# Performance work log

Hardware: AMD Instinct MI355X
Metric: run time of the kernel (lower is better)

The kernel has to match this reference:

```python
import jax, jax.numpy as jnp
import numpy as np

T, S, N, E, H, FF = 1024, 2048, 4, 1024, 16, 4096
HD = E // H
EPS = 1e-5


def layer_norm(x, g, b):
    mu = jnp.mean(x, axis=-1, keepdims=True)
    var = jnp.mean(jnp.square(x - mu), axis=-1, keepdims=True)
    return (x - mu) / jnp.sqrt(var + EPS) * g + b


def mha(q_in, k_in, v_in, w_in, b_in, w_out, b_out):
    # q_in: (T,N,E), k_in/v_in: (S,N,E); matches torch F.linear with (3E,E) weight
    t, n, e = q_in.shape
    s = k_in.shape[0]
    wq, wk, wv = jnp.split(w_in, 3, axis=0)
    bq, bk, bv = jnp.split(b_in, 3)
    q = (q_in @ wq.T + bq) * (HD ** -0.5)
    k = k_in @ wk.T + bk
    v = v_in @ wv.T + bv
    # (L,N,E) -> (N*H, L, HD)
    q = q.reshape(t, n * H, HD).transpose(1, 0, 2)
    k = k.reshape(s, n * H, HD).transpose(1, 0, 2)
    v = v.reshape(s, n * H, HD).transpose(1, 0, 2)
    attn = jax.nn.softmax(jnp.einsum('bth,bsh->bts', q, k), axis=-1)
    out = jnp.einsum('bts,bsh->bth', attn, v)  # (N*H, T, HD)
    out = out.transpose(1, 0, 2).reshape(t, n, e)
    return out @ w_out.T + b_out


def setup_inputs() -> dict:
    key = jax.random.key(0)
    ks = jax.random.split(key, 16)
    p = lambda k, shape: jax.random.normal(k, shape, dtype=jnp.float32) * 0.02
    return {
        'tgt': jax.random.normal(ks[0], (T, N, E), dtype=jnp.float32),
        'memory': jax.random.normal(ks[1], (S, N, E), dtype=jnp.float32),
        'sa_w_in': p(ks[2], (3 * E, E)), 'sa_b_in': jnp.zeros((3 * E,), jnp.float32),
        'sa_w_out': p(ks[3], (E, E)), 'sa_b_out': jnp.zeros((E,), jnp.float32),
        'ca_w_in': p(ks[4], (3 * E, E)), 'ca_b_in': jnp.zeros((3 * E,), jnp.float32),
        'ca_w_out': p(ks[5], (E, E)), 'ca_b_out': jnp.zeros((E,), jnp.float32),
        'w1': p(ks[6], (FF, E)), 'b1': jnp.zeros((FF,), jnp.float32),
        'w2': p(ks[7], (E, FF)), 'b2': jnp.zeros((E,), jnp.float32),
        'ln1_g': jnp.ones((E,), jnp.float32), 'ln1_b': jnp.zeros((E,), jnp.float32),
        'ln2_g': jnp.ones((E,), jnp.float32), 'ln2_b': jnp.zeros((E,), jnp.float32),
        'ln3_g': jnp.ones((E,), jnp.float32), 'ln3_b': jnp.zeros((E,), jnp.float32),
    }


def reference(tgt, memory, sa_w_in, sa_b_in, sa_w_out, sa_b_out,
              ca_w_in, ca_b_in, ca_w_out, ca_b_out,
              w1, b1, w2, b2, ln1_g, ln1_b, ln2_g, ln2_b, ln3_g, ln3_b):
    # self-attention block (post-LN residual); dropout = identity (eval mode)
    tgt2 = mha(tgt, tgt, tgt, sa_w_in, sa_b_in, sa_w_out, sa_b_out)
    x = layer_norm(tgt + tgt2, ln1_g, ln1_b)
    # cross-attention block
    tgt2 = mha(x, memory, memory, ca_w_in, ca_b_in, ca_w_out, ca_b_out)
    x = layer_norm(x + tgt2, ln2_g, ln2_b)
    # FFN with relu
    tgt2 = jax.nn.relu(x @ w1.T + b1) @ w2.T + b2
    return layer_norm(x + tgt2, ln3_g, ln3_b)
```

## Files before the change

kernel.cpp:

```cpp
#include <hip/hip_runtime.h>


typedef __bf16 bf16x8 __attribute__((ext_vector_type(8)));
typedef float  f32x4  __attribute__((ext_vector_type(4)));
typedef float  f32x16 __attribute__((ext_vector_type(16)));

#define T_  1024
#define S_  2048
#define NB_ 4
#define E_  1024
#define H_  16
#define HD_ 64
#define FF_ 4096
#define M1_ (T_*NB_)
#define M2_ (S_*NB_)
#define LOG2E 1.44269504088896f

__device__ __forceinline__ unsigned short f2bf(float f){
  unsigned int u = __builtin_bit_cast(unsigned int, f);
  u += 0x7fffu + ((u>>16)&1u);
  return (unsigned short)(u>>16);
}
__device__ __forceinline__ float bf2f(unsigned short h){
  unsigned int u = ((unsigned int)h)<<16;
  return __builtin_bit_cast(float, u);
}

__device__ __forceinline__ void gload16(unsigned short* l, const unsigned short* g){
  __builtin_amdgcn_global_load_lds(
      (const __attribute__((address_space(1))) unsigned int*)g,
      (__attribute__((address_space(3))) unsigned int*)l, 16, 0, 0);
}

__device__ __forceinline__ void perm32swap(unsigned &a, unsigned &b){
  asm("v_permlane32_swap_b32 %0, %1" : "+v"(a), "+v"(b));
}

struct CvtSeg { const float* s; unsigned short* d; int n4; };
struct CvtArgs { CvtSeg seg[8]; int blk_end[8]; };
__global__ __launch_bounds__(256) void f2b_multi_k(CvtArgs a){
  const int b = blockIdx.x;
  int si = 0;
  #pragma unroll
  for (int i=0;i<8;i++) if (b >= a.blk_end[i]) si = i+1;
  const int base = si ? a.blk_end[si-1] : 0;
  const int i4 = (b - base)*256 + threadIdx.x;
  if (i4 >= a.seg[si].n4) return;
  float4 f = ((const float4*)a.seg[si].s)[i4];
  union { unsigned short u[4]; uint2 v; } t;
  t.u[0]=f2bf(f.x); t.u[1]=f2bf(f.y); t.u[2]=f2bf(f.z); t.u[3]=f2bf(f.w);
  ((uint2*)a.seg[si].d)[i4] = t.v;
}

template<int FLAGS, int BN>
__global__ __launch_bounds__(256) void gemm_k(
    const unsigned short* __restrict__ A, int lda,
    const unsigned short* __restrict__ B, int ldb,
    const float* __restrict__ bias,
    const float* __restrict__ res,
    unsigned short* __restrict__ Cb, float* __restrict__ Cf,
    int M, int N, int K)
{
  constexpr int NW = BN/32;
  __shared__ unsigned short a_sh[128*64];
  __shared__ unsigned short b_sh[BN*64];
  const int tid  = threadIdx.x;
  const int wave = tid>>6;
  const int lane = tid&63;
  const int l15 = lane&15, l4 = lane>>4;
  const int row0 = blockIdx.x*128, col0 = blockIdx.y*BN;
  const int wm = (wave>>1)*64, wn = (wave&1)*(BN/2);

  const int lrow = tid>>3;
  const int scol = ((tid&7) ^ (lrow&7)) << 3;
  const int dst8 = (tid&7) << 3;

  f32x4 acc[4][NW] = {};

  for (int k0=0; k0<K; k0+=64){
    const unsigned short* ga = A + (size_t)(row0+lrow)*lda + k0 + scol;
    const unsigned short* gb = B + (size_t)(col0+lrow)*ldb + k0 + scol;
    #pragma unroll
    for (int i=0;i<4;i++)
      gload16(&a_sh[(lrow + i*32)*64 + dst8], ga + (size_t)(i*32)*lda);
    #pragma unroll
    for (int i=0;i<BN/32;i++)
      gload16(&b_sh[(lrow + i*32)*64 + dst8], gb + (size_t)(i*32)*ldb);
    __syncthreads();
    #pragma unroll
    for (int kk=0;kk<2;kk++){
      const int sw = (((kk<<2)|l4) ^ (l15&7)) << 3;
      bf16x8 af[4], bfr[NW];
      #pragma unroll
      for (int m=0;m<4;m++)  af[m]  = *(const bf16x8*)&a_sh[(wm + m*16 + l15)*64 + sw];
      #pragma unroll
      for (int n=0;n<NW;n++) bfr[n] = *(const bf16x8*)&b_sh[(wn + n*16 + l15)*64 + sw];
      #pragma unroll
      for (int m=0;m<4;m++)
        #pragma unroll
        for (int n=0;n<NW;n++)
          acc[m][n] = __builtin_amdgcn_mfma_f32_16x16x32_bf16(af[m], bfr[n], acc[m][n], 0,0,0);
    }
    __syncthreads();
  }

  #pragma unroll
  for (int m=0;m<4;m++){
    #pragma unroll
    for (int r=0;r<4;r++){
      const int rr = row0 + wm + m*16 + l4*4 + r;
      #pragma unroll
      for (int n=0;n<NW;n++){
        const int cc = col0 + wn + n*16 + l15;
        float v = acc[m][n][r] + bias[cc];
        if (FLAGS & 1) v = fmaxf(v, 0.f);
        if (FLAGS & 2) v += res[(size_t)rr*N + cc];
        if (FLAGS & 4) Cb[(size_t)rr*N + cc] = f2bf(v);
        if (FLAGS & 8) Cf[(size_t)rr*N + cc] = v;
      }
    }
  }
}

template<int BN>
__global__ __launch_bounds__(256) void gemm_splitk_k(
    const unsigned short* __restrict__ A, int lda,
    const unsigned short* __restrict__ B, int ldb,
    const float* __restrict__ bias,
    const float* __restrict__ res,
    float* __restrict__ P0, float* __restrict__ P1,
    int M, int N, int K)
{
  constexpr int NW = BN/32;
  __shared__ unsigned short a_sh[128*64];
  __shared__ unsigned short b_sh[BN*64];
  const int tid  = threadIdx.x;
  const int wave = tid>>6;
  const int lane = tid&63;
  const int l15 = lane&15, l4 = lane>>4;
  const int row0 = blockIdx.x*128, col0 = blockIdx.y*BN;
  const int wm = (wave>>1)*64, wn = (wave&1)*(BN/2);
  const int z = blockIdx.z;
  const int kh = K>>1;
  const int kbeg = z*kh;

  const int lrow = tid>>3;
  const int scol = ((tid&7) ^ (lrow&7)) << 3;
  const int dst8 = (tid&7) << 3;

  f32x4 acc[4][NW] = {};

  for (int k0=kbeg; k0<kbeg+kh; k0+=64){
    const unsigned short* ga = A + (size_t)(row0+lrow)*lda + k0 + scol;
    const unsigned short* gb = B + (size_t)(col0+lrow)*ldb + k0 + scol;
    #pragma unroll
    for (int i=0;i<4;i++)
      gload16(&a_sh[(lrow + i*32)*64 + dst8], ga + (size_t)(i*32)*lda);
    #pragma unroll
    for (int i=0;i<BN/32;i++)
      gload16(&b_sh[(lrow + i*32)*64 + dst8], gb + (size_t)(i*32)*ldb);
    __syncthreads();
    #pragma unroll
    for (int kk=0;kk<2;kk++){
      const int sw = (((kk<<2)|l4) ^ (l15&7)) << 3;
      bf16x8 af[4], bfr[NW];
      #pragma unroll
      for (int m=0;m<4;m++)  af[m]  = *(const bf16x8*)&a_sh[(wm + m*16 + l15)*64 + sw];
      #pragma unroll
      for (int n=0;n<NW;n++) bfr[n] = *(const bf16x8*)&b_sh[(wn + n*16 + l15)*64 + sw];
      #pragma unroll
      for (int m=0;m<4;m++)
        #pragma unroll
        for (int n=0;n<NW;n++)
          acc[m][n] = __builtin_amdgcn_mfma_f32_16x16x32_bf16(af[m], bfr[n], acc[m][n], 0,0,0);
    }
    __syncthreads();
  }

  float* out = z ? P1 : P0;
  #pragma unroll
  for (int m=0;m<4;m++){
    #pragma unroll
    for (int r=0;r<4;r++){
      const int rr = row0 + wm + m*16 + l4*4 + r;
      #pragma unroll
      for (int n=0;n<NW;n++){
        const int cc = col0 + wn + n*16 + l15;
        float v = acc[m][n][r];
        if (!z) v += bias[cc] + res[(size_t)rr*N + cc];
        out[(size_t)rr*N + cc] = v;
      }
    }
  }
}

template<int BN>
__global__ __launch_bounds__(256) void gemm_scat_k(
    const unsigned short* __restrict__ A, int lda,
    const unsigned short* __restrict__ B, int ldb,
    const float* __restrict__ bias,
    unsigned short* __restrict__ qb, unsigned short* __restrict__ kb,
    unsigned short* __restrict__ vtb,
    int M, int N, int K, int nq, int nk, int Lq, int Lkv, float qscale)
{
  constexpr int NW = BN/32;
  constexpr int SMEM_ELEMS = (BN==128) ? (128*132) : (128*64 + BN*64);
  __shared__ unsigned short smem[SMEM_ELEMS];
  unsigned short* a_sh = smem;
  unsigned short* b_sh = smem + 128*64;
  const int tid  = threadIdx.x;
  const int wave = tid>>6, lane = tid&63;
  const int l15 = lane&15, l4 = lane>>4;
  const int row0 = blockIdx.x*128, col0 = blockIdx.y*BN;
  const int wm = (wave>>1)*64, wn = (wave&1)*(BN/2);

  const int lrow = tid>>3;
  const int scol = ((tid&7) ^ (lrow&7)) << 3;
  const int dst8 = (tid&7) << 3;

  f32x4 acc[4][NW] = {};

  for (int k0=0; k0<K; k0+=64){
    const unsigned short* ga = A + (size_t)(row0+lrow)*lda + k0 + scol;
    const unsigned short* gb = B + (size_t)(col0+lrow)*ldb + k0 + scol;
    #pragma unroll
    for (int i=0;i<4;i++)
      gload16(&a_sh[(lrow + i*32)*64 + dst8], ga + (size_t)(i*32)*lda);
    #pragma unroll
    for (int i=0;i<BN/32;i++)
      gload16(&b_sh[(lrow + i*32)*64 + dst8], gb + (size_t)(i*32)*ldb);
    __syncthreads();
    #pragma unroll
    for (int kk=0;kk<2;kk++){
      const int sw = (((kk<<2)|l4) ^ (l15&7)) << 3;
      bf16x8 af[4], bfr[NW];
      #pragma unroll
      for (int m=0;m<4;m++)  af[m]  = *(const bf16x8*)&a_sh[(wm + m*16 + l15)*64 + sw];
      #pragma unroll
      for (int n=0;n<NW;n++) bfr[n] = *(const bf16x8*)&b_sh[(wn + n*16 + l15)*64 + sw];
      #pragma unroll
      for (int m=0;m<4;m++)
        #pragma unroll
        for (int n=0;n<NW;n++)
          acc[m][n] = __builtin_amdgcn_mfma_f32_16x16x32_bf16(af[m], bfr[n], acc[m][n], 0,0,0);
    }
    __syncthreads();
  }

  if (col0 < nq + nk){
    const bool isq = (col0 < nq);
    unsigned short* dst = isq ? qb : kb;
    const int  base  = isq ? 0 : nq;
    const int  L     = isq ? Lq : Lkv;
    const float scale = isq ? qscale : 1.0f;
    #pragma unroll
    for (int m=0;m<4;m++){
      #pragma unroll
      for (int r=0;r<4;r++){
        const int rr = row0 + wm + m*16 + l4*4 + r;
        const int t = rr>>2, nn = rr&3;
        #pragma unroll
        for (int n=0;n<NW;n++){
          const int cc = col0 + wn + n*16 + l15;
          const int e = cc - base, h = e>>6, d = e&63;
          const float v = (acc[m][n][r] + bias[cc]) * scale;
          dst[((size_t)(nn*H_ + h)*L + t)*HD_ + d] = f2bf(v);
        }
      }
    }
  } else if constexpr (BN == 128){
    unsigned short* cT = smem;
    #pragma unroll
    for (int m=0;m<4;m++){
      const int tl = ((wm + m*16)>>2) + l4;
      #pragma unroll
      for (int n=0;n<4;n++){
        const int ccl = wn + n*16 + l15;
        const float bi = bias[col0 + ccl];
        #pragma unroll
        for (int r=0;r<4;r++)
          cT[ccl*132 + r*32 + tl] = f2bf(acc[m][n][r] + bi);
      }
    }
    __syncthreads();
    const int t0 = row0>>2;
    const int tl4 = tid&7, c5 = tid>>3;
    const int voff = nq + nk;
    #pragma unroll
    for (int i=0;i<16;i++){
      const int combo = i*32 + c5;
      const int nn = combo&3, ccl = combo>>2;
      const int e = col0 + ccl - voff, h = e>>6, d = e&63;
      const uint2 val = *(const uint2*)&cT[ccl*132 + nn*32 + tl4*4];
      *(uint2*)(vtb + (size_t)((nn*H_ + h)*HD_ + d)*Lkv + t0 + tl4*4) = val;
    }
  }
}

template<bool PARTIAL, int NT>
__global__ __launch_bounds__(256,3) void attn_k(
    const unsigned short* __restrict__ qb, const unsigned short* __restrict__ kb,
    const unsigned short* __restrict__ vtb,
    unsigned short* __restrict__ o_out, float* __restrict__ l_out,
    int T, int S)
{
  static_assert((NT & 1) == 0 && NT >= 4, "NT even");
  __shared__ unsigned short k_sh[2][64*64];
  __shared__ unsigned short v_sh[2][64*64];
  __shared__ float bc_sh[4][32];
  const int tid  = threadIdx.x;
  const int wave = tid>>6, lane = tid&63;
  const int l31  = lane&31;
  const int hv   = lane>>5;
  const int bh   = blockIdx.x;
  const int z    = blockIdx.z;
  const int s_begin = z * (NT*64);
  const int q0   = blockIdx.y*128 + wave*32;
  const size_t qbase = (size_t)bh*T*HD_;
  const size_t kbase = (size_t)bh*S*HD_;
  const size_t vbase = (size_t)bh*HD_*S;

  const int strow = tid>>3;
  const int stch  = tid&7;
  const int sc_sw = (stch ^ (strow&7)) << 3;
  const int dst8  = stch<<3;
  const unsigned short* gk0 = kb  + kbase + (size_t)s_begin*HD_;
  const unsigned short* gv0 = vtb + vbase + s_begin;

  auto stageK = [&](int t, int slot){
    const unsigned short* g = gk0 + (size_t)(t*64)*HD_;
    gload16(&k_sh[slot][(strow   )*64 + dst8], g + (size_t)(strow   )*HD_ + sc_sw);
    gload16(&k_sh[slot][(strow+32)*64 + dst8], g + (size_t)(strow+32)*HD_ + sc_sw);
  };
  auto stageV = [&](int t, int slot){
    const unsigned short* g = gv0 + t*64;
    gload16(&v_sh[slot][(strow   )*64 + dst8], g + (size_t)(strow   )*S + sc_sw);
    gload16(&v_sh[slot][(strow+32)*64 + dst8], g + (size_t)(strow+32)*S + sc_sw);
  };

  bf16x8 qf[4];
  #pragma unroll
  for (int p=0;p<4;p++)
    qf[p] = *(const bf16x8*)(qb + qbase + (size_t)(q0 + l31)*HD_ + p*16 + hv*8);
  asm volatile("" ::: "memory");

  stageK(0, 0);

  f32x16 o0 = {}, o1 = {};
  float rsa = 0.f, rsb = 0.f;
  bf16x8 paA[4], paB[4];

  auto QK = [&](const unsigned short* ksh, f32x16& s0, f32x16& s1){
    #pragma unroll
    for (int p=0;p<4;p++){
      const int slot = 2*p + hv;
      bf16x8 kf0 = *(const bf16x8*)&ksh[(l31     )*64 + ((slot ^ (l31&7))<<3)];
      bf16x8 kf1 = *(const bf16x8*)&ksh[(l31 + 32)*64 + ((slot ^ (l31&7))<<3)];
      s0 = __builtin_amdgcn_mfma_f32_32x32x16_bf16(kf0, qf[p], s0, 0,0,0);
      s1 = __builtin_amdgcn_mfma_f32_32x32x16_bf16(kf1, qf[p], s1, 0,0,0);
    }
  };
  auto PV = [&](const unsigned short* vsh, const bf16x8* pa){
    #pragma unroll
    for (int ks=0;ks<4;ks++){
      const int slot = 2*ks + hv;
      bf16x8 vf0 = *(const bf16x8*)&vsh[(l31     )*64 + ((slot ^ (l31&7))<<3)];
      bf16x8 vf1 = *(const bf16x8*)&vsh[(l31 + 32)*64 + ((slot ^ (l31&7))<<3)];
      o0 = __builtin_amdgcn_mfma_f32_32x32x16_bf16(pa[ks], vf0, o0, 0,0,0);
      o1 = __builtin_amdgcn_mfma_f32_32x32x16_bf16(pa[ks], vf1, o1, 0,0,0);
    }
  };
  auto SM = [&](f32x16& s0, f32x16& s1, bf16x8* pa){
    #pragma unroll
    for (int r=0;r<16;r++){
      s0[r] = __builtin_amdgcn_exp2f(s0[r]);
      s1[r] = __builtin_amdgcn_exp2f(s1[r]);
    }
    #pragma unroll
    for (int r=0;r<16;r+=2){
      rsa += s0[r]   + s1[r];
      rsb += s0[r+1] + s1[r+1];
    }
    #pragma unroll
    for (int ks=0;ks<4;ks++){
      const int base = 8*(ks&1);
      unsigned pkA0, pkA1, pkB0, pkB1;
      if (ks < 2){
        asm("v_cvt_pk_bf16_f32 %0, %1, %2" : "=v"(pkA0) : "v"(s0[base+0]), "v"(s0[base+1]));
        asm("v_cvt_pk_bf16_f32 %0, %1, %2" : "=v"(pkA1) : "v"(s0[base+2]), "v"(s0[base+3]));
        asm("v_cvt_pk_bf16_f32 %0, %1, %2" : "=v"(pkB0) : "v"(s0[base+4]), "v"(s0[base+5]));
        asm("v_cvt_pk_bf16_f32 %0, %1, %2" : "=v"(pkB1) : "v"(s0[base+6]), "v"(s0[base+7]));
      } else {
        asm("v_cvt_pk_bf16_f32 %0, %1, %2" : "=v"(pkA0) : "v"(s1[base+0]), "v"(s1[base+1]));
        asm("v_cvt_pk_bf16_f32 %0, %1, %2" : "=v"(pkA1) : "v"(s1[base+2]), "v"(s1[base+3]));
        asm("v_cvt_pk_bf16_f32 %0, %1, %2" : "=v"(pkB0) : "v"(s1[base+4]), "v"(s1[base+5]));
        asm("v_cvt_pk_bf16_f32 %0, %1, %2" : "=v"(pkB1) : "v"(s1[base+6]), "v"(s1[base+7]));
      }
      perm32swap(pkA0, pkB0);
      perm32swap(pkA1, pkB1);
      union { unsigned w[4]; bf16x8 v; } u;
      u.w[0] = pkA0; u.w[1] = pkA1; u.w[2] = pkB0; u.w[3] = pkB1;
      pa[ks] = u.v;
    }
  };

  {
    stageK(1, 1);
    stageV(0, 0);
    asm volatile("s_waitcnt vmcnt(4)" ::: "memory");
    __builtin_amdgcn_s_barrier();
    f32x16 s0 = {}, s1 = {};
    __builtin_amdgcn_s_setprio(1);
    QK(k_sh[0], s0, s1);
    __builtin_amdgcn_s_setprio(0);
    SM(s0, s1, paA);
    __builtin_amdgcn_s_barrier();
  }

  auto BODY = [&](int i, const bf16x8* paPrev, bf16x8* paCur){
    const int kt = (i+1 < NT) ? (i+1) : (NT-1);
    stageK(kt, (i+1)&1);
    stageV(i, i&1);
    asm volatile("s_waitcnt vmcnt(4)" ::: "memory");
    __builtin_amdgcn_s_barrier();
    f32x16 s0 = {}, s1 = {};
    __builtin_amdgcn_s_setprio(1);
    QK(k_sh[i&1], s0, s1);
    PV(v_sh[(i+1)&1], paPrev);
    __builtin_amdgcn_s_setprio(0);
    SM(s0, s1, paCur);
    __builtin_amdgcn_s_barrier();
  };

  for (int ii=1; ii+1<NT; ii+=2){
    BODY(ii,   paA, paB);
    BODY(ii+1, paB, paA);
  }
  BODY(NT-1, paA, paB);

  asm volatile("s_waitcnt vmcnt(0)" ::: "memory");
  __builtin_amdgcn_s_barrier();
  __builtin_amdgcn_s_setprio(1);
  PV(v_sh[(NT-1)&1], paB);
  __builtin_amdgcn_s_setprio(0);

  float l_run = rsa + rsb;
  {
    unsigned a_ = __builtin_bit_cast(unsigned, l_run), b_ = a_;
    perm32swap(a_, b_);
    l_run += __builtin_bit_cast(float, hv ? a_ : b_);
  }

  if constexpr (PARTIAL){
    const size_t obase = (size_t)(z*64 + bh)*T;
    #pragma unroll
    for (int r=0;r<16;r++){
      const int qr = (r&3) + 8*(r>>2) + 4*hv;
      unsigned short* op = o_out + (obase + q0 + qr)*HD_;
      op[l31]      = f2bf(o0[r]);
      op[l31 + 32] = f2bf(o1[r]);
    }
    if (hv == 0) l_out[obase + q0 + l31] = l_run;
  } else {
    bc_sh[wave][l31] = 1.f / l_run;
    const int nb = bh>>4, hh = bh&15;
    #pragma unroll
    for (int r=0;r<16;r++){
      const int qr  = (r&3) + 8*(r>>2) + 4*hv;
      const float inv = bc_sh[wave][qr];
      const int t = q0 + qr;
      unsigned short* op = o_out + ((size_t)t*NB_ + nb)*E_ + hh*HD_;
      op[l31]      = f2bf(o0[r]*inv);
      op[l31 + 32] = f2bf(o1[r]*inv);
    }
  }
}

__global__ __launch_bounds__(256) void comb_k(
    const unsigned short* __restrict__ opart, const float* __restrict__ lpart,
    unsigned short* __restrict__ outb, int T)
{
  const int bh = blockIdx.y;
  const int t  = blockIdx.x*4 + (threadIdx.x>>6);
  const int d  = threadIdx.x&63;
  const size_t half = (size_t)64*T;
  const size_t row  = (size_t)bh*T + t;
  const float o = bf2f(opart[row*HD_ + d]) + bf2f(opart[(half + row)*HD_ + d]);
  const float l = lpart[row] + lpart[half + row];
  const int nb = bh>>4, hh = bh&15;
  outb[((size_t)t*NB_ + nb)*E_ + hh*HD_ + d] = f2bf(o / l);
}

__global__ __launch_bounds__(256) void ln_k(
    const float* __restrict__ p0, const float* __restrict__ p1,
    const float* __restrict__ g, const float* __restrict__ bb,
    float* __restrict__ of, unsigned short* __restrict__ ob)
{
  const int row = blockIdx.x, tid = threadIdx.x;
  const size_t base = (size_t)row*E_;
  float v[4];
  #pragma unroll
  for (int i=0;i<4;i++){
    const int col = tid + 256*i;
    v[i] = p0[base + col] + p1[base + col];
  }
  float s  = v[0]+v[1]+v[2]+v[3];
  float s2 = v[0]*v[0]+v[1]*v[1]+v[2]*v[2]+v[3]*v[3];
  #pragma unroll
  for (int off=32; off>0; off>>=1){
    s  += __shfl_down(s, off);
    s2 += __shfl_down(s2, off);
  }
  __shared__ float red[8];
  if ((tid&63)==0){ red[tid>>6] = s; red[4+(tid>>6)] = s2; }
  __syncthreads();
  s  = red[0]+red[1]+red[2]+red[3];
  s2 = red[4]+red[5]+red[6]+red[7];
  const float mu   = s * (1.f/E_);
  const float var  = s2 * (1.f/E_) - mu*mu;
  const float rstd = rsqrtf(var + 1e-5f);
  #pragma unroll
  for (int i=0;i<4;i++){
    const int col = tid + 256*i;
    const float y = (v[i]-mu)*rstd*g[col] + bb[col];
    if (of) of[base + col] = y;
    if (ob) ob[base + col] = f2bf(y);
  }
}

extern "C" void kernel_launch(void* const* d_in, const int* in_sizes, int n_in,
                              void* d_out, int out_size, void* d_ws, size_t ws_size,
                              hipStream_t stream)
{
  const float* tgt      = (const float*)d_in[0];
  const float* mem      = (const float*)d_in[1];
  const float* sa_w_in  = (const float*)d_in[2];
  const float* sa_b_in  = (const float*)d_in[3];
  const float* sa_w_out = (const float*)d_in[4];
  const float* sa_b_out = (const float*)d_in[5];
  const float* ca_w_in  = (const float*)d_in[6];
  const float* ca_b_in  = (const float*)d_in[7];
  const float* ca_w_out = (const float*)d_in[8];
  const float* ca_b_out = (const float*)d_in[9];
  const float* w1 = (const float*)d_in[10];
  const float* b1 = (const float*)d_in[11];
  const float* w2 = (const float*)d_in[12];
  const float* b2 = (const float*)d_in[13];
  const float* ln1_g=(const float*)d_in[14]; const float* ln1_b=(const float*)d_in[15];
  const float* ln2_g=(const float*)d_in[16]; const float* ln2_b=(const float*)d_in[17];
  const float* ln3_g=(const float*)d_in[18]; const float* ln3_b=(const float*)d_in[19];

  char* ws = (char*)d_ws;
  size_t off = 0;
  auto alloc = [&](size_t bytes)->char* {
    char* p = ws + off; off += (bytes + 255) & ~(size_t)255; return p;
  };
  unsigned short* w_sa_in_b  = (unsigned short*)alloc((size_t)3*E_*E_*2);
  unsigned short* w_sa_out_b = (unsigned short*)alloc((size_t)E_*E_*2);
  unsigned short* w_ca_in_b  = (unsigned short*)alloc((size_t)3*E_*E_*2);
  unsigned short* w_ca_out_b = (unsigned short*)alloc((size_t)E_*E_*2);
  unsigned short* w1_b  = (unsigned short*)alloc((size_t)FF_*E_*2);
  unsigned short* w2_b  = (unsigned short*)alloc((size_t)E_*FF_*2);
  unsigned short* tgt_b = (unsigned short*)alloc((size_t)M1_*E_*2);
  unsigned short* mem_b = (unsigned short*)alloc((size_t)M2_*E_*2);
  unsigned short* qbuf  = (unsigned short*)alloc((size_t)64*T_*HD_*2);
  unsigned short* kbuf  = (unsigned short*)alloc((size_t)64*S_*HD_*2);
  unsigned short* vtbuf = (unsigned short*)alloc((size_t)64*S_*HD_*2);
  unsigned short* cbuf  = (unsigned short*)alloc((size_t)M1_*FF_*2);
  unsigned short* atto  = (unsigned short*)alloc((size_t)M1_*E_*2);
  unsigned short* opart = (unsigned short*)alloc((size_t)2*64*T_*HD_*2);
  float*          lpart = (float*)alloc((size_t)2*64*T_*4);
  float* resf = (float*)alloc((size_t)M1_*E_*4);
  float* xf   = (float*)alloc((size_t)M1_*E_*4);
  unsigned short* xb = (unsigned short*)alloc((size_t)M1_*E_*2);
  (void)ws_size; (void)in_sizes; (void)n_in; (void)out_size;

  float* P1 = (float*)opart;

  const float QSCALE = 0.125f * LOG2E;

  {
    CvtArgs a;
    const float* srcs[8] = {tgt, mem, sa_w_in, sa_w_out, ca_w_in, ca_w_out, w1, w2};
    unsigned short* dsts[8] = {tgt_b, mem_b, w_sa_in_b, w_sa_out_b, w_ca_in_b, w_ca_out_b, w1_b, w2_b};
    size_t ns[8] = {(size_t)M1_*E_, (size_t)M2_*E_, (size_t)3*E_*E_, (size_t)E_*E_,
                    (size_t)3*E_*E_, (size_t)E_*E_, (size_t)FF_*E_, (size_t)E_*FF_};
    int blk = 0;
    for (int i=0;i<8;i++){
      a.seg[i].s = srcs[i]; a.seg[i].d = dsts[i]; a.seg[i].n4 = (int)(ns[i]/4);
      blk += (a.seg[i].n4 + 255)/256;
      a.blk_end[i] = blk;
    }
    f2b_multi_k<<<blk, 256, 0, stream>>>(a);
  }

  gemm_scat_k<128><<<dim3(M1_/128, (3*E_)/128), 256, 0, stream>>>(
      tgt_b, E_, w_sa_in_b, E_, sa_b_in, qbuf, kbuf, vtbuf,
      M1_, 3*E_, E_, E_, E_, T_, T_, QSCALE);
  attn_k<false,16><<<dim3(64, T_/128, 1), 256, 0, stream>>>(
      qbuf, kbuf, vtbuf, atto, nullptr, T_, T_);
  gemm_splitk_k<64><<<dim3(M1_/128, E_/64, 2), 256, 0, stream>>>(
      atto, E_, w_sa_out_b, E_, sa_b_out, tgt, resf, P1, M1_, E_, E_);
  ln_k<<<M1_, 256, 0, stream>>>(resf, P1, ln1_g, ln1_b, xf, xb);

  gemm_scat_k<128><<<dim3(M2_/128, (2*E_)/128), 256, 0, stream>>>(
      mem_b, E_, w_ca_in_b + (size_t)E_*E_, E_, ca_b_in + E_, nullptr, kbuf, vtbuf,
      M2_, 2*E_, E_, 0, E_, T_, S_, QSCALE);
  gemm_scat_k<64><<<dim3(M1_/128, E_/64), 256, 0, stream>>>(
      xb, E_, w_ca_in_b, E_, ca_b_in, qbuf, nullptr, nullptr,
      M1_, E_, E_, E_, 0, T_, S_, QSCALE);
  attn_k<true,16><<<dim3(64, T_/128, 2), 256, 0, stream>>>(
      qbuf, kbuf, vtbuf, opart, lpart, T_, S_);
  comb_k<<<dim3(T_/4, 64), 256, 0, stream>>>(opart, lpart, atto, T_);
  gemm_splitk_k<64><<<dim3(M1_/128, E_/64, 2), 256, 0, stream>>>(
      atto, E_, w_ca_out_b, E_, ca_b_out, xf, resf, P1, M1_, E_, E_);
  ln_k<<<M1_, 256, 0, stream>>>(resf, P1, ln2_g, ln2_b, xf, xb);

  gemm_k<5,128><<<dim3(M1_/128, FF_/128), 256, 0, stream>>>(
      xb, E_, w1_b, E_, b1, nullptr, cbuf, nullptr, M1_, FF_, E_);
  gemm_splitk_k<64><<<dim3(M1_/128, E_/64, 2), 256, 0, stream>>>(
      cbuf, FF_, w2_b, FF_, b2, xf, resf, P1, M1_, E_, FF_);
  ln_k<<<M1_, 256, 0, stream>>>(resf, P1, ln3_g, ln3_b, (float*)d_out, nullptr);
}
```

Measured before the change: 390.4 us.

## Add 256x256-tile eight-wave pipelined GEMM for FFN first layer

Introduces a new bf16 GEMM kernel with 256x256 block tiles, eight waves, a four-slot swizzled LDS ring filled by direct global-to-LDS loads, and interleaved prefetch with MFMA issue under raised wave priority. It replaces the 128x128 GEMM used for the FFN up-projection with relu. The goal is higher data reuse and better overlap of loads with matrix math. It uses 128KB of LDS, which limits occupancy to one block per CU, and the epilogue writes scattered bf16 values.

Measured after the change: 389.1 us. Within noise of the previous version (-0.3%).

```diff
diff --git a/kernel.cpp b/kernel.cpp
--- a/kernel.cpp
+++ b/kernel.cpp
@@ -36,6 +36,10 @@
   asm("v_permlane32_swap_b32 %0, %1" : "+v"(a), "+v"(b));
 }
 
+__device__ __forceinline__ int loff(int row, int kc){
+  return ((row>>1)<<6) + (((((row&1)<<2)|kc) ^ ((row>>1)&7))<<3);
+}
+
 struct CvtSeg { const float* s; unsigned short* d; int n4; };
 struct CvtArgs { CvtSeg seg[8]; int blk_end[8]; };
 __global__ __launch_bounds__(256) void f2b_multi_k(CvtArgs a){
@@ -50,6 +54,107 @@
   union { unsigned short u[4]; uint2 v; } t;
   t.u[0]=f2bf(f.x); t.u[1]=f2bf(f.y); t.u[2]=f2bf(f.z); t.u[3]=f2bf(f.w);
   ((uint2*)a.seg[si].d)[i4] = t.v;
+}
+
+template<int FLAGS>
+__global__ __launch_bounds__(512, 2) void gemm8_k(
+    const unsigned short* __restrict__ A, int lda,
+    const unsigned short* __restrict__ B, int ldb,
+    const float* __restrict__ bias,
+    unsigned short* __restrict__ Cb,
+    int M, int N, int K)
+{
+  __shared__ unsigned short a_sh[4][256*32];
+  __shared__ unsigned short b_sh[4][256*32];
+  const int tid  = threadIdx.x;
+  const int wave = tid>>6, lane = tid&63;
+  const int l15 = lane&15, l4 = lane>>4;
+
+  int bid = blockIdx.x;
+  if ((gridDim.x & 7) == 0){ const int cpx = gridDim.x>>3; bid = (bid&7)*cpx + (bid>>3); }
+  const int nbm = M>>8;
+  const int bm = bid % nbm, bn = bid / nbm;
+  const int brow = bm<<8, bcol = bn<<8;
+  const int wm0 = (wave>>2)*128, wn = (wave&3)*64;
+  const int NT = K>>5;
+
+  int ldsl[2]; const unsigned short* pA[2]; const unsigned short* pB[2];
+  #pragma unroll
+  for (int i=0;i<2;i++){
+    const int l = i*512 + wave*64 + lane;
+    const int grp = l>>3, sl = (l&7) ^ (grp&7);
+    const int row = (grp<<1)|(sl>>2), c = sl&3;
+    ldsl[i] = l<<3;
+    pA[i] = A + (size_t)(brow + row)*lda + (c<<3);
+    pB[i] = B + (size_t)(bcol + row)*ldb + (c<<3);
+  }
+
+  f32x4 acc[8][4] = {};
+
+  auto stageA = [&](int t){
+    unsigned short* s = a_sh[t&3];
+    #pragma unroll
+    for (int i=0;i<2;i++) gload16(&s[ldsl[i]], pA[i] + t*32);
+  };
+  auto stageB = [&](int t){
+    unsigned short* s = b_sh[t&3];
+    #pragma unroll
+    for (int i=0;i<2;i++) gload16(&s[ldsl[i]], pB[i] + t*32);
+  };
+
+  stageA(0); stageB(0); stageA(1); stageB(1);
+  asm volatile("s_waitcnt vmcnt(4)" ::: "memory");
+  __builtin_amdgcn_s_barrier();
+
+  for (int t=0; t<NT; ++t){
+    const unsigned short* as = a_sh[t&3];
+    const unsigned short* bs = b_sh[t&3];
+    const bool pre = (t+2 < NT);
+
+    if (pre) stageA(t+2);
+    bf16x8 bf[4], af[4];
+    #pragma unroll
+    for (int n=0;n<4;n++) bf[n] = *(const bf16x8*)&bs[loff(wn + n*16 + l15, l4)];
+    #pragma unroll
+    for (int m=0;m<4;m++) af[m] = *(const bf16x8*)&as[loff(wm0 + m*16 + l15, l4)];
+    __builtin_amdgcn_s_setprio(1);
+    #pragma unroll
+    for (int m=0;m<4;m++)
+      #pragma unroll
+      for (int n=0;n<4;n++)
+        acc[m][n] = __builtin_amdgcn_mfma_f32_16x16x32_bf16(af[m], bf[n], acc[m][n], 0,0,0);
+    __builtin_amdgcn_s_setprio(0);
+    __builtin_amdgcn_s_barrier();
+
+    if (pre) stageB(t+2);
+    #pragma unroll
+    for (int m=0;m<4;m++) af[m] = *(const bf16x8*)&as[loff(wm0 + 64 + m*16 + l15, l4)];
+    __builtin_amdgcn_s_setprio(1);
+    #pragma unroll
+    for (int m=0;m<4;m++)
+      #pragma unroll
+      for (int n=0;n<4;n++)
+        acc[4+m][n] = __builtin_amdgcn_mfma_f32_16x16x32_bf16(af[m], bf[n], acc[4+m][n], 0,0,0);
+    __builtin_amdgcn_s_setprio(0);
+    if (pre) asm volatile("s_waitcnt vmcnt(4)" ::: "memory");
+    else     asm volatile("s_waitcnt vmcnt(0)" ::: "memory");
+    __builtin_amdgcn_s_barrier();
+  }
+
+  #pragma unroll
+  for (int mi=0;mi<8;mi++){
+    #pragma unroll
+    for (int r=0;r<4;r++){
+      const int rr = brow + wm0 + mi*16 + l4*4 + r;
+      #pragma unroll
+      for (int n=0;n<4;n++){
+        const int cc = bcol + wn + n*16 + l15;
+        float v = acc[mi][n][r] + bias[cc];
+        if (FLAGS & 1) v = fmaxf(v, 0.f);
+        Cb[(size_t)rr*N + cc] = f2bf(v);
+      }
+    }
+  }
 }
 
 template<int FLAGS, int BN>
@@ -616,8 +721,8 @@
       atto, E_, w_ca_out_b, E_, ca_b_out, xf, resf, P1, M1_, E_, E_);
   ln_k<<<M1_, 256, 0, stream>>>(resf, P1, ln2_g, ln2_b, xf, xb);
 
-  gemm_k<5,128><<<dim3(M1_/128, FF_/128), 256, 0, stream>>>(
-      xb, E_, w1_b, E_, b1, nullptr, cbuf, nullptr, M1_, FF_, E_);
+  gemm8_k<5><<<(M1_/256)*(FF_/256), 512, 0, stream>>>(
+      xb, E_, w1_b, E_, b1, cbuf, M1_, FF_, E_);
   gemm_splitk_k<64><<<dim3(M1_/128, E_/64, 2), 256, 0, stream>>>(
       cbuf, FF_, w2_b, FF_, b2, xf, resf, P1, M1_, E_, FF_);
   ln_k<<<M1_, 256, 0, stream>>>(resf, P1, ln3_g, ln3_b, (float*)d_out, nullptr);
```
